# Performance work log

Hardware: AMD Instinct MI355X
Metric: run time of the kernel (lower is better)

Reference implementation:

```python
import jax, jax.numpy as jnp
import numpy as np

N = 16384       # structure nodes
H = 256         # in_channels == hidden_channels
E_BOLD = 524288
E_TEMP = 262144
T_ATTR = 107    # hardcoded in temporal_edge_proj Linear(107, hidden)
EPS = 1e-5


def layer_norm(x, g, b):
    m = x.mean(-1, keepdims=True)
    v = ((x - m) ** 2).mean(-1, keepdims=True)
    return (x - m) * jax.lax.rsqrt(v + EPS) * g + b


def gcn_conv(x, W, b, edge_index, edge_weight):
    """PyG GCNConv: add self-loops (weight 1), symmetric normalization,
    out_i = sum_j norm_ij * (x_j @ W) + b."""
    n = x.shape[0]
    loop = jnp.arange(n)
    row = jnp.concatenate([edge_index[0], loop])   # source
    col = jnp.concatenate([edge_index[1], loop])   # target
    w = jnp.concatenate([edge_weight, jnp.ones((n,), x.dtype)])
    deg = jax.ops.segment_sum(w, col, num_segments=n)
    dis = jnp.where(deg > 0, jax.lax.rsqrt(jnp.where(deg > 0, deg, 1.0)), 0.0)
    norm = dis[row] * w * dis[col]
    h = x @ W                                       # [n, H]
    out = jax.ops.segment_sum(norm[:, None] * h[row], col, num_segments=n)
    return out + b


def setup_inputs() -> dict:
    key = jax.random.key(0)
    ks = jax.random.split(key, 12)
    s = 1.0 / np.sqrt(H)
    return {
        "x_struct": jax.random.normal(ks[0], (N, H), jnp.float32),
        "bold_edge_index": jax.random.randint(ks[1], (2, E_BOLD), 0, N),
        "bold_edge_weight": jax.random.uniform(ks[2], (E_BOLD,), jnp.float32),
        "temp_edge_index": jax.random.randint(ks[3], (2, E_TEMP), 0, N),
        "temp_edge_attr": jax.random.normal(ks[4], (E_TEMP, T_ATTR), jnp.float32),
        "W_bold": jax.random.normal(ks[5], (H, H), jnp.float32) * s,
        "b_bold": jnp.zeros((H,), jnp.float32),
        "W_temp": jax.random.normal(ks[6], (H, H), jnp.float32) * s,
        "b_temp": jnp.zeros((H,), jnp.float32),
        "ln_struct_g": jnp.ones((H,), jnp.float32),
        "ln_struct_b": jnp.zeros((H,), jnp.float32),
        "ln_temp_g": jnp.ones((H,), jnp.float32),
        "ln_temp_b": jnp.zeros((H,), jnp.float32),
        "proj_w1": jax.random.normal(ks[7], (T_ATTR, H), jnp.float32) / np.sqrt(T_ATTR),
        "proj_b1": jnp.zeros((H,), jnp.float32),
        "proj_g": jnp.ones((H,), jnp.float32),
        "proj_beta": jnp.zeros((H,), jnp.float32),
        "proj_w2": jax.random.normal(ks[8], (H, 1), jnp.float32) * 0.01,
        "proj_b2": jnp.ones((1,), jnp.float32),  # keeps temporal edge weights > 0 (valid GCN norm)
    }


def reference(x_struct, bold_edge_index, bold_edge_weight, temp_edge_index,
              temp_edge_attr, W_bold, b_bold, W_temp, b_temp,
              ln_struct_g, ln_struct_b, ln_temp_g, ln_temp_b,
              proj_w1, proj_b1, proj_g, proj_beta, proj_w2, proj_b2):
    s0 = x_struct
    # bold GCN + residual + struct_norm + relu
    bold_out = gcn_conv(s0, W_bold, b_bold, bold_edge_index, bold_edge_weight)
    s = jax.nn.relu(layer_norm(bold_out + s0, ln_struct_g, ln_struct_b))
    # temporal edge-attr MLP -> scalar edge weight (temporal_dim == 1)
    h = jax.nn.relu(layer_norm(temp_edge_attr @ proj_w1 + proj_b1, proj_g, proj_beta))
    temp_w = (h @ proj_w2 + proj_b2)[:, 0]          # [E_TEMP]
    # temporal GCN + residual + temporal_norm + relu
    temporal_out = gcn_conv(s, W_temp, b_temp, temp_edge_index, temp_w)
    s = jax.nn.relu(layer_norm(temporal_out + s, ln_temp_g, ln_temp_b))
    # final residual to original features through struct_norm
    return layer_norm(s + s0, ln_struct_g, ln_struct_b)
```

## Files before the change

### kernel.cpp

```cpp
#include <hip/hip_runtime.h>

constexpr int kN  = 16384;
constexpr int kEB = 524288;
constexpr int kET = 262144;
constexpr int kTA = 107;
constexpr float kEps = 1e-5f;
#define HN 256

typedef __attribute__((ext_vector_type(8))) short short8;
typedef __attribute__((ext_vector_type(4))) float floatx4;
typedef unsigned short u16;
typedef unsigned int u32;

#define GLOAD_LDS16(gp, lp)                                                    \
  __builtin_amdgcn_global_load_lds(                                            \
      (const __attribute__((address_space(1))) u32*)(gp),                      \
      (__attribute__((address_space(3))) u32*)(lp), 16, 0, 0)

__device__ __forceinline__ u32 bf16rn(float f) {
  u32 u = __float_as_uint(f);
  return (u + 0x7FFFu + ((u >> 16) & 1u)) >> 16;
}
__device__ __forceinline__ u32 pack2(float a, float b) {
  return bf16rn(a) | (bf16rn(b) << 16);
}
__device__ __forceinline__ float bf2f(u32 v) {
  return __uint_as_float(v << 16);
}
__device__ __forceinline__ u32 cvtpk(float lo, float hi) {
  u32 r;
  asm("v_cvt_pk_bf16_f32 %0, %1, %2" : "=v"(r) : "v"(lo), "v"(hi));
  return r;
}
__device__ __forceinline__ void ub8(uint4 u, float* f) {
  f[0] = bf2f(u.x & 0xFFFF); f[1] = bf2f(u.x >> 16);
  f[2] = bf2f(u.y & 0xFFFF); f[3] = bf2f(u.y >> 16);
  f[4] = bf2f(u.z & 0xFFFF); f[5] = bf2f(u.z >> 16);
  f[6] = bf2f(u.w & 0xFFFF); f[7] = bf2f(u.w >> 16);
}
__device__ __forceinline__ u32 swz512(u32 b) { return b ^ (((b >> 9) & 7u) << 4); }

__global__ __launch_bounds__(256)
void k_prep_const(const float* __restrict__ w1, const float* __restrict__ Wb,
                  const float* __restrict__ Wt, const float* __restrict__ b1,
                  const float* __restrict__ pg, const float* __restrict__ pbeta,
                  const float* __restrict__ w2, u16* __restrict__ pk1,
                  u16* __restrict__ pkb, u16* __restrict__ pkt,
                  float4* __restrict__ pp, const float* __restrict__ x,
                  u16* __restrict__ xb, uint4* __restrict__ zero4) {
  int bid = blockIdx.x, tid = threadIdx.x;
  if (bid < 641) {
    int idx = bid * 256 + tid;
    if (idx < 32768) {
      int e = idx & 7, lane = (idx >> 3) & 63, ct = (idx >> 9) & 15, kk = idx >> 13;
      int k = kk * 32 + (lane >> 4) * 8 + e, col = ct * 16 + (lane & 15);
      pk1[idx] = (u16)(k < kTA ? bf16rn(w1[(size_t)k * 256 + col]) : 0);
    } else if (idx < 163840) {
      int j = idx - 32768;
      const float* W = (j < 65536) ? Wb : Wt;
      u16* pk = (j < 65536) ? pkb : pkt;
      int t = j & 65535;
      int e = t & 7, lane = (t >> 3) & 63, ct = (t >> 9) & 15, kt = t >> 13;
      int k = kt * 32 + (lane >> 4) * 8 + e, col = ct * 16 + (lane & 15);
      pk[t] = (u16)bf16rn(W[(size_t)k * 256 + col]);
    } else if (idx < 163840 + 256) {
      int col = idx - 163840;
      pp[col] = make_float4(b1[col], pg[col], pbeta[col], w2[col]);
    }
  } else if (bid < 641 + 2048) {
    size_t i = (size_t)((bid - 641) * 256 + tid) * 8;
    float4 a = *(const float4*)(x + i);
    float4 b = *(const float4*)(x + i + 4);
    *(uint4*)(xb + i) = make_uint4(pack2(a.x, a.y), pack2(a.z, a.w),
                                   pack2(b.x, b.y), pack2(b.z, b.w));
  } else {
    zero4[(bid - 2689) * 256 + tid] = make_uint4(0, 0, 0, 0);
  }
}

#define PROJ_TILES 4
__global__ __launch_bounds__(512)
void k_proj_mfma(const float* __restrict__ attr, const u16* __restrict__ pk1,
                 const float* __restrict__ b1, const float4* __restrict__ pp,
                 const float* __restrict__ b2, float* __restrict__ temp_w) {
  __shared__ __align__(16) u16 Btile[32768];
  int tid = threadIdx.x;
  int w = tid >> 6, lane = tid & 63, low4 = lane & 15, hi = lane >> 4;

#pragma unroll
  for (int it = 0; it < 8; ++it) {
    int chunk = it * 512 + tid;
    GLOAD_LDS16((const char*)pk1 + (size_t)chunk * 16,
                (char*)Btile + (it * 512 + w * 64) * 16);
  }

  auto buildA = [&](int t, short8* a) {
    int e0 = (blockIdx.x * PROJ_TILES + t) * 128 + w * 16;
    const float* rowp = attr + (size_t)(e0 + low4) * kTA;
#pragma unroll
    for (int kk = 0; kk < 4; ++kk) {
      int kb = kk * 32 + hi * 8;
      float v[8];
#pragma unroll
      for (int e = 0; e < 8; ++e)
        v[e] = (kk < 3 || kb + e < kTA) ? rowp[kb + e] : 0.f;
      union { short8 s8; uint4 u4; } fr;
      fr.u4 = make_uint4(cvtpk(v[0], v[1]), cvtpk(v[2], v[3]),
                         cvtpk(v[4], v[5]), cvtpk(v[6], v[7]));
      a[kk] = fr.s8;
    }
  };

  short8 a_cur[4];
  buildA(0, a_cur);
  float b2s = b2[0];

  __syncthreads();

#pragma unroll
  for (int t = 0; t < PROJ_TILES; ++t) {
    int e0 = (blockIdx.x * PROJ_TILES + t) * 128 + w * 16;
    short8 a_next[4];
    if (t + 1 < PROJ_TILES) buildA(t + 1, a_next);

    u32 hvpk[16][2];
    float s1[4] = {0.f, 0.f, 0.f, 0.f}, s2[4] = {0.f, 0.f, 0.f, 0.f};
#pragma unroll
    for (int nn = 0; nn < 16; ++nn) {
      floatx4 acc = (floatx4){0.f, 0.f, 0.f, 0.f};
#pragma unroll
      for (int kk = 0; kk < 4; ++kk) {
        short8 bfr = *(const short8*)(Btile + ((size_t)(kk * 16 + nn) * 64 + lane) * 8);
        acc = __builtin_amdgcn_mfma_f32_16x16x32_bf16(a_cur[kk], bfr, acc, 0, 0, 0);
      }
      float b1v = b1[nn * 16 + low4];
      float h0 = acc[0] + b1v, h1 = acc[1] + b1v, h2 = acc[2] + b1v, h3 = acc[3] + b1v;
      s1[0] += h0; s2[0] += h0 * h0;
      s1[1] += h1; s2[1] += h1 * h1;
      s1[2] += h2; s2[2] += h2 * h2;
      s1[3] += h3; s2[3] += h3 * h3;
      hvpk[nn][0] = cvtpk(h0, h1);
      hvpk[nn][1] = cvtpk(h2, h3);
    }

    float mean[4], inv[4];
#pragma unroll
    for (int j = 0; j < 4; ++j) {
#pragma unroll
      for (int m = 1; m < 16; m <<= 1) {
        s1[j] += __shfl_xor(s1[j], m, 64);
        s2[j] += __shfl_xor(s2[j], m, 64);
      }
      mean[j] = s1[j] * (1.f / 256);
      inv[j] = rsqrtf(s2[j] * (1.f / 256) - mean[j] * mean[j] + kEps);
    }

    float d[4] = {0.f, 0.f, 0.f, 0.f};
#pragma unroll
    for (int nn = 0; nn < 16; ++nn) {
      float4 p = pp[nn * 16 + low4];
      float h0 = bf2f(hvpk[nn][0] & 0xFFFF);
      float h1 = bf2f(hvpk[nn][0] >> 16);
      float h2 = bf2f(hvpk[nn][1] & 0xFFFF);
      float h3 = bf2f(hvpk[nn][1] >> 16);
      d[0] += fmaxf((h0 - mean[0]) * inv[0] * p.y + p.z, 0.f) * p.w;
      d[1] += fmaxf((h1 - mean[1]) * inv[1] * p.y + p.z, 0.f) * p.w;
      d[2] += fmaxf((h2 - mean[2]) * inv[2] * p.y + p.z, 0.f) * p.w;
      d[3] += fmaxf((h3 - mean[3]) * inv[3] * p.y + p.z, 0.f) * p.w;
    }
#pragma unroll
    for (int j = 0; j < 4; ++j) {
#pragma unroll
      for (int m = 1; m < 16; m <<= 1) d[j] += __shfl_xor(d[j], m, 64);
      if (low4 == 0) temp_w[e0 + hi * 4 + j] = d[j] + b2s;
    }
#pragma unroll
    for (int kk = 0; kk < 4; ++kk) a_cur[kk] = a_next[kk];
  }
}

__device__ __forceinline__
void gemm_role(u16* Atile, const u16* __restrict__ Ab,
               const u16* __restrict__ pkW, u16* __restrict__ Cb, int gid) {
  int tid = threadIdx.x;
  int w = tid >> 6, lane = tid & 63, low4 = lane & 15, hi = lane >> 4;
  int row0 = gid * 32;

  const char* asrc = (const char*)(Ab + (size_t)row0 * 256);
#pragma unroll
  for (int i = 0; i < 4; ++i) {
    u32 d = (u32)(((i * 4 + w) * 64 + lane) * 16);
    GLOAD_LDS16(asrc + swz512(d), (char*)Atile + (i * 4 + w) * 1024);
  }

  floatx4 acc[2][4];
#pragma unroll
  for (int rt = 0; rt < 2; ++rt)
#pragma unroll
    for (int nn = 0; nn < 4; ++nn) acc[rt][nn] = (floatx4){0.f, 0.f, 0.f, 0.f};

  __syncthreads();

#pragma unroll
  for (int kt = 0; kt < 8; ++kt) {
    short8 bfr[4];
    const u16* pw = pkW + ((size_t)(kt * 16 + w * 4) * 64 + lane) * 8;
#pragma unroll
    for (int nn = 0; nn < 4; ++nn) bfr[nn] = *(const short8*)(pw + nn * 512);
    short8 afr[2];
#pragma unroll
    for (int rt = 0; rt < 2; ++rt) {
      u32 p = (u32)((rt * 16 + low4) * 512 + (kt * 32 + hi * 8) * 2);
      afr[rt] = *(const short8*)((const char*)Atile + swz512(p));
    }
#pragma unroll
    for (int rt = 0; rt < 2; ++rt)
#pragma unroll
      for (int nn = 0; nn < 4; ++nn)
        acc[rt][nn] = __builtin_amdgcn_mfma_f32_16x16x32_bf16(afr[rt], bfr[nn],
                                                              acc[rt][nn], 0, 0, 0);
  }
#pragma unroll
  for (int rt = 0; rt < 2; ++rt)
#pragma unroll
    for (int nn = 0; nn < 4; ++nn)
#pragma unroll
      for (int j = 0; j < 4; ++j) {
        int row = row0 + rt * 16 + hi * 4 + j;
        int col = w * 64 + nn * 16 + low4;
        Cb[(size_t)row * 256 + col] = (u16)bf16rn(acc[rt][nn][j]);
      }
}

__global__ __launch_bounds__(256)
void k_gemm1_prepb(const u16* __restrict__ xb, const u16* __restrict__ pkb,
                   u16* __restrict__ hb, const int* __restrict__ bcol,
                   const float* __restrict__ bw, float* __restrict__ deg_b,
                   int* __restrict__ cnt_b) {
  __shared__ __align__(16) u16 Atile[32 * 256];
  int bid = blockIdx.x;
  int r = bid >> 8, idx = bid & 255;
  if (r < 2) {
    gemm_role(Atile, xb, pkb, hb, r * 256 + idx);
  } else {
    int e = ((r - 2) * 256 + idx) * 256 + threadIdx.x;
    int c = bcol[e];
    atomicAdd(&deg_b[c], bw[e]);
    atomicAdd(&cnt_b[c], 1);
  }
}

__device__ __forceinline__
void scan_role(const int* __restrict__ cnt, int* __restrict__ base,
               int* __restrict__ cur, const float* __restrict__ deg,
               float* __restrict__ dis) {
  __shared__ int part[256];
  int tid = threadIdx.x;
  int per = kN >> 8;
  int i0 = tid * per;
  int s = 0;
  for (int k = 0; k < per; ++k) s += cnt[i0 + k];
  part[tid] = s;
  __syncthreads();
  for (int off = 1; off < 256; off <<= 1) {
    int v = (tid >= off) ? part[tid - off] : 0;
    __syncthreads();
    part[tid] += v;
    __syncthreads();
  }
  int run = (tid == 0) ? 0 : part[tid - 1];
  for (int k = 0; k < per; ++k) {
    base[i0 + k] = run; cur[i0 + k] = run; run += cnt[i0 + k];
    float d = deg[i0 + k] + 1.0f;
    dis[i0 + k] = (d > 0.f) ? rsqrtf(d) : 0.f;
  }
  if (tid == 255) base[kN] = run;
}

template <int FINAL>
__device__ __forceinline__
void agg_role(const u16* __restrict__ h, const void* __restrict__ residv,
              const float* __restrict__ x0, const int2* __restrict__ csr,
              const int* __restrict__ basep, const float* __restrict__ dis,
              const float* __restrict__ bias, const float* __restrict__ g1,
              const float* __restrict__ b1, const float* __restrict__ g2,
              const float* __restrict__ b2, void* __restrict__ outv, int aid) {
  int tid = threadIdx.x;
  int sub = tid >> 5, lane = tid & 31;
  int node = aid * 8 + sub;
  int c = lane * 8;
  const u16* hcol = h + c;
  float di = dis[node];
  float sl = di * di;
  float acc[8];
  {
    uint4 u = *(const uint4*)(hcol + (size_t)node * HN);
    float f[8]; ub8(u, f);
#pragma unroll
    for (int i = 0; i < 8; ++i) acc[i] = f[i] * sl;
  }
  int e0 = basep[node], e1 = basep[node + 1];
  int k = e0;
  for (; k + 4 <= e1; k += 4) {
    int2 p0 = csr[k], p1 = csr[k + 1], p2 = csr[k + 2], p3 = csr[k + 3];
    uint4 u0 = *(const uint4*)(hcol + (size_t)p0.x * HN);
    uint4 u1 = *(const uint4*)(hcol + (size_t)p1.x * HN);
    uint4 u2 = *(const uint4*)(hcol + (size_t)p2.x * HN);
    uint4 u3 = *(const uint4*)(hcol + (size_t)p3.x * HN);
    float n0 = __int_as_float(p0.y), n1 = __int_as_float(p1.y);
    float n2 = __int_as_float(p2.y), n3 = __int_as_float(p3.y);
    float f0[8], f1[8], f2[8], f3[8];
    ub8(u0, f0); ub8(u1, f1); ub8(u2, f2); ub8(u3, f3);
#pragma unroll
    for (int i = 0; i < 8; ++i)
      acc[i] += n0 * f0[i] + n1 * f1[i] + n2 * f2[i] + n3 * f3[i];
  }
  for (; k < e1; ++k) {
    int2 p = csr[k];
    uint4 u = *(const uint4*)(hcol + (size_t)p.x * HN);
    float nf = __int_as_float(p.y);
    float f[8]; ub8(u, f);
#pragma unroll
    for (int i = 0; i < 8; ++i) acc[i] += nf * f[i];
  }
  float v[8];
  {
    float4 b0 = *(const float4*)(bias + c);
    float4 b4 = *(const float4*)(bias + c + 4);
    float bb[8] = {b0.x, b0.y, b0.z, b0.w, b4.x, b4.y, b4.z, b4.w};
    float rr[8];
    if (!FINAL) {
      const float* rp = (const float*)residv + (size_t)node * HN + c;
      float4 r0 = *(const float4*)rp;
      float4 r4 = *(const float4*)(rp + 4);
      rr[0] = r0.x; rr[1] = r0.y; rr[2] = r0.z; rr[3] = r0.w;
      rr[4] = r4.x; rr[5] = r4.y; rr[6] = r4.z; rr[7] = r4.w;
    } else {
      uint4 u = *(const uint4*)((const u16*)residv + (size_t)node * HN + c);
      ub8(u, rr);
    }
#pragma unroll
    for (int i = 0; i < 8; ++i) v[i] = acc[i] + bb[i] + rr[i];
  }
  float s1 = 0.f, s2 = 0.f;
#pragma unroll
  for (int i = 0; i < 8; ++i) { s1 += v[i]; s2 += v[i] * v[i]; }
#pragma unroll
  for (int m = 1; m < 32; m <<= 1) {
    s1 += __shfl_xor(s1, m, 64);
    s2 += __shfl_xor(s2, m, 64);
  }
  float mean = s1 * (1.f / HN);
  float inv = rsqrtf(s2 * (1.f / HN) - mean * mean + kEps);
  float4 ga = *(const float4*)(g1 + c);
  float4 gb = *(const float4*)(g1 + c + 4);
  float4 ba = *(const float4*)(b1 + c);
  float4 bbv = *(const float4*)(b1 + c + 4);
  float gg[8] = {ga.x, ga.y, ga.z, ga.w, gb.x, gb.y, gb.z, gb.w};
  float bt[8] = {ba.x, ba.y, ba.z, ba.w, bbv.x, bbv.y, bbv.z, bbv.w};
  float y[8];
#pragma unroll
  for (int i = 0; i < 8; ++i)
    y[i] = fmaxf((v[i] - mean) * inv * gg[i] + bt[i], 0.f);
  if (!FINAL) {
    uint4 o = make_uint4(cvtpk(y[0], y[1]), cvtpk(y[2], y[3]),
                         cvtpk(y[4], y[5]), cvtpk(y[6], y[7]));
    *(uint4*)((u16*)outv + (size_t)node * HN + c) = o;
  } else {
    const float* xp = x0 + (size_t)node * HN + c;
    float4 x0v = *(const float4*)xp;
    float4 x4v = *(const float4*)(xp + 4);
    float xx[8] = {x0v.x, x0v.y, x0v.z, x0v.w, x4v.x, x4v.y, x4v.z, x4v.w};
    float z[8];
    float t1 = 0.f, t2 = 0.f;
#pragma unroll
    for (int i = 0; i < 8; ++i) {
      z[i] = y[i] + xx[i];
      t1 += z[i]; t2 += z[i] * z[i];
    }
#pragma unroll
    for (int m = 1; m < 32; m <<= 1) {
      t1 += __shfl_xor(t1, m, 64);
      t2 += __shfl_xor(t2, m, 64);
    }
    float m2 = t1 * (1.f / HN);
    float i2 = rsqrtf(t2 * (1.f / HN) - m2 * m2 + kEps);
    float4 Ga = *(const float4*)(g2 + c);
    float4 Gb = *(const float4*)(g2 + c + 4);
    float4 Ba = *(const float4*)(b2 + c);
    float4 Bb = *(const float4*)(b2 + c + 4);
    float G[8] = {Ga.x, Ga.y, Ga.z, Ga.w, Gb.x, Gb.y, Gb.z, Gb.w};
    float B[8] = {Ba.x, Ba.y, Ba.z, Ba.w, Bb.x, Bb.y, Bb.z, Bb.w};
    float* op = (float*)outv + (size_t)node * HN + c;
    *(float4*)op = make_float4((z[0] - m2) * i2 * G[0] + B[0],
                               (z[1] - m2) * i2 * G[1] + B[1],
                               (z[2] - m2) * i2 * G[2] + B[2],
                               (z[3] - m2) * i2 * G[3] + B[3]);
    *(float4*)(op + 4) = make_float4((z[4] - m2) * i2 * G[4] + B[4],
                                     (z[5] - m2) * i2 * G[5] + B[5],
                                     (z[6] - m2) * i2 * G[6] + B[6],
                                     (z[7] - m2) * i2 * G[7] + B[7]);
  }
}

__global__ __launch_bounds__(256)
void k_scanb_prept(const int* __restrict__ cnt_b, int* __restrict__ base_b,
                   int* __restrict__ cur_b, const float* __restrict__ deg_b,
                   float* __restrict__ dis_b, const int* __restrict__ tcol,
                   const float* __restrict__ tmpw, float* __restrict__ deg_t,
                   int* __restrict__ cnt_t) {
  if (blockIdx.x == 0) {
    scan_role(cnt_b, base_b, cur_b, deg_b, dis_b);
  } else {
    int eid = (blockIdx.x - 1) * 256 + threadIdx.x;
    int c = tcol[eid];
    atomicAdd(&deg_t[c], tmpw[eid]);
    atomicAdd(&cnt_t[c], 1);
  }
}

__global__ __launch_bounds__(256)
void k_fillb_scant(const int* __restrict__ bei, const float* __restrict__ bw,
                   const float* __restrict__ dis_b, int* __restrict__ cur_b,
                   int2* __restrict__ csr_b, const int* __restrict__ cnt_t,
                   int* __restrict__ base_t, int* __restrict__ cur_t,
                   const float* __restrict__ deg_t, float* __restrict__ dis_t) {
  if (blockIdx.x == 0) {
    scan_role(cnt_t, base_t, cur_t, deg_t, dis_t);
  } else {
    int eid = (blockIdx.x - 1) * 256 + threadIdx.x;
    int rr = bei[eid], c = bei[kEB + eid];
    float nrm = dis_b[rr] * bw[eid] * dis_b[c];
    int pos = atomicAdd(&cur_b[c], 1);
    csr_b[pos] = make_int2(rr, __float_as_int(nrm));
  }
}

__global__ __launch_bounds__(256)
void k_agg0_fillt(const u16* __restrict__ hb, const float* __restrict__ x,
                  const int2* __restrict__ csr_b, const int* __restrict__ base_b,
                  const float* __restrict__ dis_b, const float* __restrict__ bbias,
                  const float* __restrict__ gs, const float* __restrict__ bs,
                  u16* __restrict__ sb, const int* __restrict__ tei,
                  const float* __restrict__ tmpw, const float* __restrict__ dis_t,
                  int* __restrict__ cur_t, int2* __restrict__ csr_t) {
  int bid = blockIdx.x;
  int r = bid >> 8, idx = bid & 255;
  if (r % 3 == 1) {
    int eid = ((r / 3) * 256 + idx) * 256 + threadIdx.x;
    int rr = tei[eid], c = tei[kET + eid];
    float nrm = dis_t[rr] * tmpw[eid] * dis_t[c];
    int pos = atomicAdd(&cur_t[c], 1);
    csr_t[pos] = make_int2(rr, __float_as_int(nrm));
  } else {
    int agg_ord = r - r / 3 - (r % 3 == 2 ? 1 : 0);
    agg_role<0>(hb, x, nullptr, csr_b, base_b, dis_b, bbias, gs, bs,
                nullptr, nullptr, sb, agg_ord * 256 + idx);
  }
}

__global__ __launch_bounds__(256)
void k_gemm_mfma(const u16* __restrict__ Ab, const u16* __restrict__ pkW,
                 u16* __restrict__ Cb) {
  __shared__ __align__(16) u16 Atile[32 * 256];
  gemm_role(Atile, Ab, pkW, Cb, blockIdx.x);
}

__global__ __launch_bounds__(256)
void k_agg1(const u16* __restrict__ h, const u16* __restrict__ sb,
            const float* __restrict__ x0, const int2* __restrict__ csr,
            const int* __restrict__ basep, const float* __restrict__ dis,
            const float* __restrict__ bias, const float* __restrict__ g1,
            const float* __restrict__ b1, const float* __restrict__ g2,
            const float* __restrict__ b2, float* __restrict__ outp) {
  agg_role<1>(h, sb, x0, csr, basep, dis, bias, g1, b1, g2, b2, outp, blockIdx.x);
}

extern "C" void kernel_launch(void* const* d_in, const int* in_sizes, int n_in,
                              void* d_out, int out_size, void* d_ws, size_t ws_size,
                              hipStream_t stream) {
  const float* x     = (const float*)d_in[0];
  const int*   bei   = (const int*)d_in[1];
  const float* bew   = (const float*)d_in[2];
  const int*   tei   = (const int*)d_in[3];
  const float* tattr = (const float*)d_in[4];
  const float* Wb    = (const float*)d_in[5];
  const float* bb    = (const float*)d_in[6];
  const float* Wt    = (const float*)d_in[7];
  const float* bt    = (const float*)d_in[8];
  const float* gs    = (const float*)d_in[9];
  const float* bs    = (const float*)d_in[10];
  const float* gt    = (const float*)d_in[11];
  const float* btn   = (const float*)d_in[12];
  const float* pw1   = (const float*)d_in[13];
  const float* pb1   = (const float*)d_in[14];
  const float* pg    = (const float*)d_in[15];
  const float* pbeta = (const float*)d_in[16];
  const float* pw2   = (const float*)d_in[17];
  const float* pb2   = (const float*)d_in[18];
  float* outp = (float*)d_out;

  size_t off = 0;
  auto alloc = [&](size_t bytes) -> void* {
    void* p = (char*)d_ws + off;
    off += (bytes + 255) & ~(size_t)255;
    return p;
  };
  float* deg_b = (float*)alloc(kN * 4);
  float* deg_t = (float*)alloc(kN * 4);
  int*   cnt_b = (int*)alloc(kN * 4);
  int*   cnt_t = (int*)alloc(kN * 4);
  float* dis_b = (float*)alloc(kN * 4);
  float* dis_t = (float*)alloc(kN * 4);
  int*   base_b = (int*)alloc((kN + 1) * 4);
  int*   base_t = (int*)alloc((kN + 1) * 4);
  int*   cur_b  = (int*)alloc(kN * 4);
  int*   cur_t  = (int*)alloc(kN * 4);
  float* tmpw   = (float*)alloc(kET * 4);
  int2*  csr_b  = (int2*)alloc((size_t)kEB * 8);
  int2*  csr_t  = (int2*)alloc((size_t)kET * 8);
  u16*   pk1 = (u16*)alloc(32768 * 2);
  u16*   pkb = (u16*)alloc(65536 * 2);
  u16*   pkt = (u16*)alloc(65536 * 2);
  float4* pp = (float4*)alloc(256 * 16);
  u16*   xb  = (u16*)alloc((size_t)kN * HN * 2);
  u16*   hb  = (u16*)alloc((size_t)kN * HN * 2);
  u16*   sb  = (u16*)alloc((size_t)kN * HN * 2);
  (void)ws_size; (void)in_sizes; (void)n_in; (void)out_size;

  k_prep_const<<<2753, 256, 0, stream>>>(pw1, Wb, Wt, pb1, pg, pbeta, pw2,
                                         pk1, pkb, pkt, pp, x, xb,
                                         (uint4*)deg_b);
  k_proj_mfma<<<kET / 128 / PROJ_TILES, 512, 0, stream>>>(tattr, pk1, pb1, pp,
                                                          pb2, tmpw);
  k_gemm1_prepb<<<2560, 256, 0, stream>>>(xb, pkb, hb, bei + kEB, bew,
                                          deg_b, cnt_b);
  k_scanb_prept<<<1 + kET / 256, 256, 0, stream>>>(cnt_b, base_b, cur_b, deg_b,
                                                   dis_b, tei + kET, tmpw,
                                                   deg_t, cnt_t);
  k_fillb_scant<<<1 + kEB / 256, 256, 0, stream>>>(bei, bew, dis_b, cur_b, csr_b,
                                                   cnt_t, base_t, cur_t,
                                                   deg_t, dis_t);
  k_agg0_fillt<<<3072, 256, 0, stream>>>(hb, x, csr_b, base_b, dis_b, bb, gs, bs,
                                         sb, tei, tmpw, dis_t, cur_t, csr_t);
  k_gemm_mfma<<<kN / 32, 256, 0, stream>>>(sb, pkt, hb);
  k_agg1<<<kN / 8, 256, 0, stream>>>(hb, sb, x, csr_t, base_t, dis_t,
                                     bt, gt, btn, gs, bs, outp);
}
```

Measured before the change: 257.7 us.

## Regroup independent stages to merge three launches into two fused kernels

The bold-degree atomic counting now runs inside the temporal projection kernel as extra blocks. The bold scan, the first GEMM and the temporal-degree counting share one kernel with interleaved block roles. This removes a kernel launch and the serialization between dependent phases, and lets atomic-heavy blocks overlap with MFMA blocks. The risk is worse occupancy, because the atomic blocks now carry the large LDS footprint and 512-thread launch of the projection kernel. A single scan block also runs alongside the GEMM.

```diff
diff --git a/kernel.cpp b/kernel.cpp
--- a/kernel.cpp
+++ b/kernel.cpp
@@ -80,11 +80,25 @@
 
 #define PROJ_TILES 4
 __global__ __launch_bounds__(512)
-void k_proj_mfma(const float* __restrict__ attr, const u16* __restrict__ pk1,
-                 const float* __restrict__ b1, const float4* __restrict__ pp,
-                 const float* __restrict__ b2, float* __restrict__ temp_w) {
+void k_proj_prepb(const float* __restrict__ attr, const u16* __restrict__ pk1,
+                  const float* __restrict__ b1, const float4* __restrict__ pp,
+                  const float* __restrict__ b2, float* __restrict__ temp_w,
+                  const int* __restrict__ bcol, const float* __restrict__ bw,
+                  float* __restrict__ deg_b, int* __restrict__ cnt_b) {
   __shared__ __align__(16) u16 Btile[32768];
-  int tid = threadIdx.x;
+  int bid = blockIdx.x, tid = threadIdx.x;
+  int r = bid >> 8, idx = bid & 255;
+
+  if (r == 1 || r >= 3) {
+    int prepord = (r == 1) ? 0 : r - 2;
+    int e = (prepord * 256 + idx) * 512 + tid;
+    int c = bcol[e];
+    atomicAdd(&deg_b[c], bw[e]);
+    atomicAdd(&cnt_b[c], 1);
+    return;
+  }
+  int projid = idx + (r == 2 ? 256 : 0);
+
   int w = tid >> 6, lane = tid & 63, low4 = lane & 15, hi = lane >> 4;
 
 #pragma unroll
@@ -95,7 +109,7 @@
   }
 
   auto buildA = [&](int t, short8* a) {
-    int e0 = (blockIdx.x * PROJ_TILES + t) * 128 + w * 16;
+    int e0 = (projid * PROJ_TILES + t) * 128 + w * 16;
     const float* rowp = attr + (size_t)(e0 + low4) * kTA;
 #pragma unroll
     for (int kk = 0; kk < 4; ++kk) {
@@ -119,7 +133,7 @@
 
 #pragma unroll
   for (int t = 0; t < PROJ_TILES; ++t) {
-    int e0 = (blockIdx.x * PROJ_TILES + t) * 128 + w * 16;
+    int e0 = (projid * PROJ_TILES + t) * 128 + w * 16;
     short8 a_next[4];
     if (t + 1 < PROJ_TILES) buildA(t + 1, a_next);
 
@@ -232,29 +246,10 @@
       }
 }
 
-__global__ __launch_bounds__(256)
-void k_gemm1_prepb(const u16* __restrict__ xb, const u16* __restrict__ pkb,
-                   u16* __restrict__ hb, const int* __restrict__ bcol,
-                   const float* __restrict__ bw, float* __restrict__ deg_b,
-                   int* __restrict__ cnt_b) {
-  __shared__ __align__(16) u16 Atile[32 * 256];
-  int bid = blockIdx.x;
-  int r = bid >> 8, idx = bid & 255;
-  if (r < 2) {
-    gemm_role(Atile, xb, pkb, hb, r * 256 + idx);
-  } else {
-    int e = ((r - 2) * 256 + idx) * 256 + threadIdx.x;
-    int c = bcol[e];
-    atomicAdd(&deg_b[c], bw[e]);
-    atomicAdd(&cnt_b[c], 1);
-  }
-}
-
 __device__ __forceinline__
 void scan_role(const int* __restrict__ cnt, int* __restrict__ base,
                int* __restrict__ cur, const float* __restrict__ deg,
-               float* __restrict__ dis) {
-  __shared__ int part[256];
+               float* __restrict__ dis, int* part) {
   int tid = threadIdx.x;
   int per = kN >> 8;
   int i0 = tid * per;
@@ -275,6 +270,31 @@
     dis[i0 + k] = (d > 0.f) ? rsqrtf(d) : 0.f;
   }
   if (tid == 255) base[kN] = run;
+}
+
+__global__ __launch_bounds__(256)
+void k_gemm1_l3(const u16* __restrict__ xb, const u16* __restrict__ pkb,
+                u16* __restrict__ hb, const int* __restrict__ cnt_b,
+                int* __restrict__ base_b, int* __restrict__ cur_b,
+                const float* __restrict__ deg_b, float* __restrict__ dis_b,
+                const int* __restrict__ tcol, const float* __restrict__ tmpw,
+                float* __restrict__ deg_t, int* __restrict__ cnt_t) {
+  __shared__ __align__(16) u16 Atile[32 * 256];
+  int bid = blockIdx.x;
+  if (bid == 1536) {
+    scan_role(cnt_b, base_b, cur_b, deg_b, dis_b, (int*)Atile);
+    return;
+  }
+  int r = bid >> 8, idx = bid & 255;
+  if (r == 0 || r == 2) {
+    gemm_role(Atile, xb, pkb, hb, idx + (r == 2 ? 256 : 0));
+  } else {
+    int prepord = (r == 1) ? 0 : r - 2;
+    int eid = (prepord * 256 + idx) * 256 + threadIdx.x;
+    int c = tcol[eid];
+    atomicAdd(&deg_t[c], tmpw[eid]);
+    atomicAdd(&cnt_t[c], 1);
+  }
 }
 
 template <int FINAL>
@@ -404,29 +424,14 @@
 }
 
 __global__ __launch_bounds__(256)
-void k_scanb_prept(const int* __restrict__ cnt_b, int* __restrict__ base_b,
-                   int* __restrict__ cur_b, const float* __restrict__ deg_b,
-                   float* __restrict__ dis_b, const int* __restrict__ tcol,
-                   const float* __restrict__ tmpw, float* __restrict__ deg_t,
-                   int* __restrict__ cnt_t) {
-  if (blockIdx.x == 0) {
-    scan_role(cnt_b, base_b, cur_b, deg_b, dis_b);
-  } else {
-    int eid = (blockIdx.x - 1) * 256 + threadIdx.x;
-    int c = tcol[eid];
-    atomicAdd(&deg_t[c], tmpw[eid]);
-    atomicAdd(&cnt_t[c], 1);
-  }
-}
-
-__global__ __launch_bounds__(256)
 void k_fillb_scant(const int* __restrict__ bei, const float* __restrict__ bw,
                    const float* __restrict__ dis_b, int* __restrict__ cur_b,
                    int2* __restrict__ csr_b, const int* __restrict__ cnt_t,
                    int* __restrict__ base_t, int* __restrict__ cur_t,
                    const float* __restrict__ deg_t, float* __restrict__ dis_t) {
+  __shared__ int part[256];
   if (blockIdx.x == 0) {
-    scan_role(cnt_t, base_t, cur_t, deg_t, dis_t);
+    scan_role(cnt_t, base_t, cur_t, deg_t, dis_t, part);
   } else {
     int eid = (blockIdx.x - 1) * 256 + threadIdx.x;
     int rr = bei[eid], c = bei[kEB + eid];
@@ -531,13 +536,11 @@
   k_prep_const<<<2753, 256, 0, stream>>>(pw1, Wb, Wt, pb1, pg, pbeta, pw2,
                                          pk1, pkb, pkt, pp, x, xb,
                                          (uint4*)deg_b);
-  k_proj_mfma<<<kET / 128 / PROJ_TILES, 512, 0, stream>>>(tattr, pk1, pb1, pp,
-                                                          pb2, tmpw);
-  k_gemm1_prepb<<<2560, 256, 0, stream>>>(xb, pkb, hb, bei + kEB, bew,
-                                          deg_b, cnt_b);
-  k_scanb_prept<<<1 + kET / 256, 256, 0, stream>>>(cnt_b, base_b, cur_b, deg_b,
-                                                   dis_b, tei + kET, tmpw,
-                                                   deg_t, cnt_t);
+  k_proj_prepb<<<1536, 512, 0, stream>>>(tattr, pk1, pb1, pp, pb2, tmpw,
+                                         bei + kEB, bew, deg_b, cnt_b);
+  k_gemm1_l3<<<1537, 256, 0, stream>>>(xb, pkb, hb, cnt_b, base_b, cur_b,
+                                       deg_b, dis_b, tei + kET, tmpw,
+                                       deg_t, cnt_t);
   k_fillb_scant<<<1 + kEB / 256, 256, 0, stream>>>(bei, bew, dis_b, cur_b, csr_b,
                                                    cnt_t, base_t, cur_t,
                                                    deg_t, dis_t);
```

Result: no change. 256.1 us (-0.6%).
